# Optimization experiments

Measured on AMD Instinct MI355X. Metric: run time of the kernel, lower is better.

The kernel has to match this reference:

```python
import jax, jax.numpy as jnp
import numpy as np

NUM_GROUPS = 32
EPS = 1e-6


def group_norm(x, gamma, beta):
    # x: [b, c, h, w]
    b, c, h, w = x.shape
    g = NUM_GROUPS
    xg = x.reshape(b, g, c // g, h, w)
    mean = jnp.mean(xg, axis=(2, 3, 4), keepdims=True)
    var = jnp.var(xg, axis=(2, 3, 4), keepdims=True)
    xg = (xg - mean) * jax.lax.rsqrt(var + EPS)
    x = xg.reshape(b, c, h, w)
    return x * gamma[None, :, None, None] + beta[None, :, None, None]


def conv1x1(x, w, bias):
    # x: [b, c_in, h, w], w: [c_out, c_in], bias: [c_out]
    return jnp.einsum('bihw,oi->bohw', x, w) + bias[None, :, None, None]


def setup_inputs() -> dict:
    key = jax.random.key(0)
    ks = jax.random.split(key, 10)
    c = 512
    b, h, w = 4, 64, 64
    scale = 1.0 / np.sqrt(c)
    inp = {
        'x': jax.random.normal(ks[0], (b, c, h, w), dtype=jnp.float32),
        'gn_gamma': jnp.ones((c,), dtype=jnp.float32),
        'gn_beta': jnp.zeros((c,), dtype=jnp.float32),
        'wq': jax.random.normal(ks[1], (c, c), dtype=jnp.float32) * scale,
        'bq': jnp.zeros((c,), dtype=jnp.float32),
        'wk': jax.random.normal(ks[2], (c, c), dtype=jnp.float32) * scale,
        'bk': jnp.zeros((c,), dtype=jnp.float32),
        'wv': jax.random.normal(ks[3], (c, c), dtype=jnp.float32) * scale,
        'bv': jnp.zeros((c,), dtype=jnp.float32),
        'wo': jax.random.normal(ks[4], (c, c), dtype=jnp.float32) * scale,
        'bo': jnp.zeros((c,), dtype=jnp.float32),
    }
    return inp


def reference(x, gn_gamma, gn_beta, wq, bq, wk, bk, wv, bv, wo, bo):
    b, c, h, w = x.shape
    h_ = group_norm(x, gn_gamma, gn_beta)
    q = conv1x1(h_, wq, bq)
    k = conv1x1(h_, wk, bk)
    v = conv1x1(h_, wv, bv)
    n = h * w
    q = q.reshape(b, c, n).transpose(0, 2, 1)  # [b, n, c]
    k = k.reshape(b, c, n)                      # [b, c, n]
    v = v.reshape(b, c, n).transpose(0, 2, 1)  # [b, n, c]
    sim = jnp.einsum('bqc,bck->bqk', q, k) * (c ** -0.5)  # [b, n, n]
    attn = jax.nn.softmax(sim, axis=-1)
    out = jnp.einsum('bqk,bkc->bqc', attn, v)  # [b, n, c]
    out = out.transpose(0, 2, 1).reshape(b, c, h, w)
    out = conv1x1(out, wo, bo)
    return x + out
```

## Files before the change

### kernel.cpp

```cpp
#include <hip/hip_runtime.h>


typedef __attribute__((ext_vector_type(8))) short bf16x8;
typedef __attribute__((ext_vector_type(4))) float f32x4;

#define MFMA16(a, b, c) __builtin_amdgcn_mfma_f32_16x16x32_bf16((a), (b), (c), 0, 0, 0)

#define B_   4
#define C_   512
#define N_   4096
#define SCALE 0.044194173824159216f
#define ESHIFT 12.0f
#define SC2   0.06376297465050853f
#define ES2   17.312340490667562f

__device__ __forceinline__ unsigned short f2bf(float f) {
    union { float f; unsigned int u; } v; v.f = f;
    unsigned int r = (v.u + 0x7fffu + ((v.u >> 16) & 1u)) >> 16;
    return (unsigned short)r;
}
__device__ __forceinline__ float bf2f(unsigned short s) {
    union { unsigned int u; float f; } v; v.u = ((unsigned int)s) << 16;
    return v.f;
}

__device__ __forceinline__ void async16(const unsigned short* g, unsigned short* l) {
    __builtin_amdgcn_global_load_lds((const __attribute__((address_space(1))) unsigned int*)g,
                                     (__attribute__((address_space(3))) unsigned int*)l,
                                     16, 0, 0);
}

__global__ __launch_bounds__(256) void gn_partial(const float* __restrict__ x,
                                                  float* __restrict__ part) {
    int blk = blockIdx.x;
    int gid = blk >> 2, qtr = blk & 3;
    const float4* base = (const float4*)(x + (size_t)gid * 65536) + qtr * 4096;
    float s = 0.f, ss = 0.f;
    for (int i = threadIdx.x; i < 4096; i += 256) {
        float4 v = base[i];
        s  += v.x + v.y + v.z + v.w;
        ss += v.x * v.x + v.y * v.y + v.z * v.z + v.w * v.w;
    }
    __shared__ float red[512];
    int t = threadIdx.x;
    red[t] = s; red[256 + t] = ss;
    __syncthreads();
    for (int st = 128; st > 0; st >>= 1) {
        if (t < st) { red[t] += red[t + st]; red[256 + t] += red[256 + t + st]; }
        __syncthreads();
    }
    if (t == 0) { part[blk] = red[0]; part[512 + blk] = red[256]; }
}

__global__ __launch_bounds__(256) void gn_apply(const float* __restrict__ x,
                                                const float* __restrict__ gamma,
                                                const float* __restrict__ beta,
                                                const float* __restrict__ part,
                                                unsigned short* __restrict__ ht) {
    __shared__ float tile[64][65];
    __shared__ float mrs[4][2];
    int j0 = blockIdx.x * 64, c0 = blockIdx.y * 64, b = blockIdx.z;
    int t = threadIdx.x;
    if (t < 4) {
        int gid = b * 32 + (c0 >> 4) + t;
        float s = 0.f, ss = 0.f;
#pragma unroll
        for (int q = 0; q < 4; ++q) { s += part[gid * 4 + q]; ss += part[512 + gid * 4 + q]; }
        float mean = s * (1.f / 65536.f);
        float var  = ss * (1.f / 65536.f) - mean * mean;
        mrs[t][0] = mean;
        mrs[t][1] = rsqrtf(var + 1e-6f);
    }
    __syncthreads();
#pragma unroll
    for (int i = 0; i < 16; ++i) {
        int lid = i * 256 + t;
        int cl = lid >> 6, jl = lid & 63;
        int c = c0 + cl;
        float v = x[((size_t)b * C_ + c) * N_ + j0 + jl];
        tile[cl][jl] = (v - mrs[cl >> 4][0]) * mrs[cl >> 4][1] * gamma[c] + beta[c];
    }
    __syncthreads();
#pragma unroll
    for (int i = 0; i < 16; ++i) {
        int lid = i * 256 + t;
        int jl = lid >> 6, cl = lid & 63;
        ht[((size_t)b * N_ + j0 + jl) * C_ + c0 + cl] = f2bf(tile[cl][jl]);
    }
}

__global__ __launch_bounds__(256) void wconv(const float* __restrict__ wq,
                                             const float* __restrict__ wk,
                                             const float* __restrict__ wv,
                                             const float* __restrict__ wo,
                                             unsigned short* __restrict__ dst) {
    size_t i = (size_t)blockIdx.x * 256 + threadIdx.x;
    int m = (int)(i >> 18);
    size_t off = i & 262143;
    const float* src = (m == 0) ? wq : (m == 1) ? wk : (m == 2) ? wv : wo;
    dst[i] = f2bf(src[off]);
}

template <typename EPI>
__device__ __forceinline__ void gemm_core(const unsigned short* __restrict__ Abase,
                                          const unsigned short* __restrict__ Bbase,
                                          size_t lda, size_t ldb, int K, EPI epi) {
    __shared__ unsigned short hl[2][128 * 64];
    __shared__ unsigned short wl[2][128 * 64];
    int t = threadIdx.x;
    int wv = t >> 6, lane = t & 63, l15 = lane & 15, quad = lane >> 4;
    int wm = wv & 1, wn = wv >> 1;
    int srow = lane >> 3;
    int sch  = ((lane & 7) ^ srow) * 8;
    int xr = l15 & 7;
    f32x4 acc[4][4] = {};
#pragma unroll
    for (int i = 0; i < 4; ++i) {
        int seg = wv * 4 + i;
        size_t row = seg * 8 + srow;
        async16(&Abase[row * lda + sch], &hl[0][seg * 512]);
        async16(&Bbase[row * ldb + sch], &wl[0][seg * 512]);
    }
    int nk = K >> 6;
    for (int k = 0; k < nk; ++k) {
        int cur = k & 1;
        __builtin_amdgcn_s_waitcnt(0x3F70);
        __syncthreads();
        if (k + 1 < nk) {
            int k0 = (k + 1) << 6;
#pragma unroll
            for (int i = 0; i < 4; ++i) {
                int seg = wv * 4 + i;
                size_t row = seg * 8 + srow;
                async16(&Abase[row * lda + k0 + sch], &hl[cur ^ 1][seg * 512]);
                async16(&Bbase[row * ldb + k0 + sch], &wl[cur ^ 1][seg * 512]);
            }
        }
#pragma unroll
        for (int kk = 0; kk < 2; ++kk) {
            int sl = (((kk << 2) + quad) ^ xr) * 8;
            bf16x8 af[4], bfr[4];
#pragma unroll
            for (int mi = 0; mi < 4; ++mi)
                af[mi] = *(const bf16x8*)&hl[cur][(wm * 64 + mi * 16 + l15) * 64 + sl];
#pragma unroll
            for (int ni = 0; ni < 4; ++ni)
                bfr[ni] = *(const bf16x8*)&wl[cur][(wn * 64 + ni * 16 + l15) * 64 + sl];
#pragma unroll
            for (int mi = 0; mi < 4; ++mi)
#pragma unroll
                for (int ni = 0; ni < 4; ++ni)
                    acc[mi][ni] = MFMA16(af[mi], bfr[ni], acc[mi][ni]);
        }
    }
    epi(acc, wm, wn, l15, quad);
}

__global__ __launch_bounds__(256) void gemm_qkv(const unsigned short* __restrict__ Ht,
                                                const unsigned short* __restrict__ Wb,
                                                const float* __restrict__ bq,
                                                const float* __restrict__ bk,
                                                const float* __restrict__ bv,
                                                unsigned short* __restrict__ Qt,
                                                unsigned short* __restrict__ Kt,
                                                unsigned short* __restrict__ Vg) {
    int b = blockIdx.z, j0 = blockIdx.x * 128;
    int ct = blockIdx.y;
    int slab = ct >> 2, co0 = (ct & 3) * 128;
    const unsigned short* A = Ht + ((size_t)b * N_ + j0) * C_;
    const unsigned short* B = Wb + (size_t)slab * C_ * C_ + (size_t)co0 * C_;
    const float* bias = (slab == 0) ? bq : (slab == 1) ? bk : bv;
    unsigned short* outqk = (slab == 0) ? Qt : Kt;
    gemm_core(A, B, C_, C_, C_,
        [&](f32x4 (&acc)[4][4], int wm, int wn, int l15, int quad) {
        if (slab < 2) {
#pragma unroll
            for (int mi = 0; mi < 4; ++mi)
#pragma unroll
                for (int ni = 0; ni < 4; ++ni)
#pragma unroll
                    for (int r = 0; r < 4; ++r) {
                        int mrow = wm * 64 + mi * 16 + quad * 4 + r;
                        int ncol = wn * 64 + ni * 16 + l15;
                        outqk[((size_t)b * N_ + j0 + mrow) * C_ + co0 + ncol] =
                            f2bf(acc[mi][ni][r] + bias[co0 + ncol]);
                    }
        } else {
#pragma unroll
            for (int mi = 0; mi < 4; ++mi)
#pragma unroll
                for (int ni = 0; ni < 4; ++ni) {
                    int ncol = wn * 64 + ni * 16 + l15;
                    float bb = bias[co0 + ncol];
                    ushort4 pk;
                    pk.x = f2bf(acc[mi][ni][0] + bb);
                    pk.y = f2bf(acc[mi][ni][1] + bb);
                    pk.z = f2bf(acc[mi][ni][2] + bb);
                    pk.w = f2bf(acc[mi][ni][3] + bb);
                    int jb = j0 + wm * 64 + mi * 16 + quad * 4;
                    *(ushort4*)&Vg[((size_t)b * C_ + co0 + ncol) * N_ + jb] = pk;
                }
        }
    });
}

__global__ __launch_bounds__(512, 2) void gemm_qk_exp(const unsigned short* __restrict__ Qt,
                                                      const unsigned short* __restrict__ Kt,
                                                      unsigned short* __restrict__ P,
                                                      float* __restrict__ psum) {
    extern __shared__ unsigned short sm[];
    int lin = blockIdx.x + 16 * blockIdx.y + 256 * blockIdx.z;
    int xcd = lin & 7;
    int i4  = lin >> 3;
    int idx = i4 & 31;
    int b   = i4 >> 5;
    int rq  = xcd & 3, rk = xcd >> 2;
    int j0  = (rq * 4 + (idx & 3)) * 256;
    int ky  = rk * 8 + (idx >> 2);
    int kc0 = ky * 256;
    const unsigned short* A  = Qt + ((size_t)b * N_ + j0) * C_;
    const unsigned short* Bm = Kt + ((size_t)b * N_ + kc0) * C_;

    int t = threadIdx.x;
    int w = t >> 6, lane = t & 63, l15 = lane & 15, quad = lane >> 4;
    int wm = w >> 2, wn = w & 3;
    int srow = lane >> 2;
    int sch  = (((lane & 3) ^ ((lane >> 3) & 3))) * 8;
    int slotq = (quad ^ ((l15 >> 1) & 3)) * 8;

    f32x4 acc[8][4] = {};

    const int NT = 16;
#pragma unroll
    for (int tt = 0; tt < 3; ++tt) {
        unsigned short* dst = sm + (tt << 14);
        size_t k0 = (size_t)tt << 5;
#pragma unroll
        for (int i = 0; i < 2; ++i) {
            int seg = w * 2 + i;
            size_t row = (size_t)seg * 16 + srow;
            async16(&A [row * C_ + k0 + sch], dst + seg * 512);
            async16(&Bm[row * C_ + k0 + sch], dst + 8192 + seg * 512);
        }
    }
    __builtin_amdgcn_s_waitcnt(0x3F78);
    __builtin_amdgcn_s_barrier();

    for (int tt = 0; tt < NT; ++tt) {
        const unsigned short* bp = sm + ((tt & 3) << 14);
        unsigned short* stg = sm + (((tt + 3) & 3) << 14);
        const bool dostage = (tt + 3 < NT);
        size_t k0n = (size_t)(tt + 3) << 5;
        bf16x8 bfr[4], af[4], af2[4];
#pragma unroll
        for (int ni = 0; ni < 4; ++ni)
            bfr[ni] = *(const bf16x8*)&bp[8192 + (wn * 64 + ni * 16 + l15) * 32 + slotq];
#pragma unroll
        for (int mi = 0; mi < 4; ++mi)
            af[mi] = *(const bf16x8*)&bp[(wm * 128 + mi * 16 + l15) * 32 + slotq];
        if (dostage) {
#pragma unroll
            for (int i = 0; i < 2; ++i) {
                int seg = w * 2 + i;
                size_t row = (size_t)seg * 16 + srow;
                async16(&A[row * C_ + k0n + sch], stg + seg * 512);
            }
        }
        __builtin_amdgcn_s_setprio(1);
#pragma unroll
        for (int mi = 0; mi < 4; ++mi)
#pragma unroll
            for (int ni = 0; ni < 4; ++ni)
                acc[mi][ni] = MFMA16(af[mi], bfr[ni], acc[mi][ni]);
        __builtin_amdgcn_s_setprio(0);
#pragma unroll
        for (int mi = 0; mi < 4; ++mi)
            af2[mi] = *(const bf16x8*)&bp[(wm * 128 + (mi + 4) * 16 + l15) * 32 + slotq];
        if (dostage) {
#pragma unroll
            for (int i = 0; i < 2; ++i) {
                int seg = w * 2 + i;
                size_t row = (size_t)seg * 16 + srow;
                async16(&Bm[row * C_ + k0n + sch], stg + 8192 + seg * 512);
            }
        }
        __builtin_amdgcn_s_setprio(1);
#pragma unroll
        for (int mi = 0; mi < 4; ++mi)
#pragma unroll
            for (int ni = 0; ni < 4; ++ni)
                acc[4 + mi][ni] = MFMA16(af2[mi], bfr[ni], acc[4 + mi][ni]);
        __builtin_amdgcn_s_setprio(0);
        if (tt + 1 < NT) {
            if (tt < NT - 3)       __builtin_amdgcn_s_waitcnt(0x3F78);
            else if (tt == NT - 3) __builtin_amdgcn_s_waitcnt(0x3F74);
            else                   __builtin_amdgcn_s_waitcnt(0x3F70);
            __builtin_amdgcn_s_barrier();
        }
    }

#pragma unroll
    for (int mi = 0; mi < 8; ++mi) {
        float rs[4] = {0.f, 0.f, 0.f, 0.f};
#pragma unroll
        for (int ni = 0; ni < 4; ++ni) {
            int ncol = kc0 + wn * 64 + ni * 16 + l15;
#pragma unroll
            for (int r = 0; r < 4; ++r) {
                int mrow = j0 + wm * 128 + mi * 16 + quad * 4 + r;
                float p = exp2f(__builtin_fmaf(acc[mi][ni][r], SC2, -ES2));
                rs[r] += p;
                P[((size_t)b * N_ + mrow) * N_ + ncol] = f2bf(p);
            }
        }
#pragma unroll
        for (int r = 0; r < 4; ++r) {
            float v = rs[r];
            v += __shfl_xor(v, 1);
            v += __shfl_xor(v, 2);
            v += __shfl_xor(v, 4);
            v += __shfl_xor(v, 8);
            if (l15 == 0)
                psum[(size_t)(wn * 16 + ky) * 16384 +
                     (size_t)b * N_ + j0 + wm * 128 + mi * 16 + quad * 4 + r] = v;
        }
    }
}

__global__ __launch_bounds__(512, 2) void gemm_pv(const unsigned short* __restrict__ P,
                                                  const unsigned short* __restrict__ Vg,
                                                  const float* __restrict__ psum,
                                                  unsigned short* __restrict__ ao) {
    extern __shared__ unsigned short sm[];
    __shared__ float linv[256];
    int lin = blockIdx.x;
    int xcd = lin & 7;
    int i4  = lin >> 3;
    int ct  = i4 & 3;
    int grp = xcd + 8 * (i4 >> 2);
    int b = grp & 3, qtile = grp >> 2;
    int j0 = qtile * 256, co0 = ct * 128;
    int t = threadIdx.x;
    int w = t >> 6, lane = t & 63, l15 = lane & 15, quad = lane >> 4;
    int wm = w >> 1, wn = w & 1;
    int srow = lane >> 2;
    int sch  = ((lane & 3) ^ ((lane >> 3) & 3)) * 8;
    int slotq = (quad ^ ((l15 >> 1) & 3)) * 8;
    const unsigned short* A  = P  + ((size_t)b * N_ + j0) * N_;
    const unsigned short* Bm = Vg + ((size_t)b * C_ + co0) * N_;
    f32x4 acc[4][4] = {};
    const int NT = 128;
#pragma unroll
    for (int tt = 0; tt < 3; ++tt) {
        unsigned short* dst = sm + tt * 12288;
        size_t k0 = (size_t)tt << 5;
#pragma unroll
        for (int i = 0; i < 2; ++i) {
            int seg = w * 2 + i;
            size_t row = (size_t)seg * 16 + srow;
            async16(&A[row * N_ + k0 + sch], dst + seg * 512);
        }
        {
            size_t row = (size_t)w * 16 + srow;
            async16(&Bm[row * N_ + k0 + sch], dst + 8192 + w * 512);
        }
    }
    if (t < 256) {
        size_t q = (size_t)b * N_ + j0 + t;
        float s = 0.f;
#pragma unroll
        for (int i = 0; i < 64; ++i) s += psum[(size_t)i * 16384 + q];
        linv[t] = 1.f / s;
    }
    __builtin_amdgcn_s_waitcnt(0x3F76);
    __builtin_amdgcn_s_barrier();
    for (int tt = 0; tt < NT; ++tt) {
        const unsigned short* bp = sm + (tt & 3) * 12288;
        bf16x8 af[4], bfr[4];
#pragma unroll
        for (int mi = 0; mi < 4; ++mi)
            af[mi] = *(const bf16x8*)&bp[(wm * 64 + mi * 16 + l15) * 32 + slotq];
#pragma unroll
        for (int ni = 0; ni < 4; ++ni)
            bfr[ni] = *(const bf16x8*)&bp[8192 + (wn * 64 + ni * 16 + l15) * 32 + slotq];
        if (tt + 3 < NT) {
            unsigned short* stg = sm + ((tt + 3) & 3) * 12288;
            size_t k0n = (size_t)(tt + 3) << 5;
#pragma unroll
            for (int i = 0; i < 2; ++i) {
                int seg = w * 2 + i;
                size_t row = (size_t)seg * 16 + srow;
                async16(&A[row * N_ + k0n + sch], stg + seg * 512);
            }
            {
                size_t row = (size_t)w * 16 + srow;
                async16(&Bm[row * N_ + k0n + sch], stg + 8192 + w * 512);
            }
        }
        __builtin_amdgcn_s_setprio(1);
#pragma unroll
        for (int mi = 0; mi < 4; ++mi)
#pragma unroll
            for (int ni = 0; ni < 4; ++ni)
                acc[mi][ni] = MFMA16(af[mi], bfr[ni], acc[mi][ni]);
        __builtin_amdgcn_s_setprio(0);
        if (tt + 1 < NT) {
            if (tt + 3 < NT)      __builtin_amdgcn_s_waitcnt(0x3F76);
            else if (tt + 2 < NT) __builtin_amdgcn_s_waitcnt(0x3F73);
            else                  __builtin_amdgcn_s_waitcnt(0x3F70);
            __builtin_amdgcn_s_barrier();
        }
    }
#pragma unroll
    for (int mi = 0; mi < 4; ++mi)
#pragma unroll
        for (int ni = 0; ni < 4; ++ni)
#pragma unroll
            for (int r = 0; r < 4; ++r) {
                int mrow = wm * 64 + mi * 16 + quad * 4 + r;
                int ncol = wn * 64 + ni * 16 + l15;
                ao[((size_t)b * N_ + j0 + mrow) * C_ + co0 + ncol] =
                    f2bf(acc[mi][ni][r] * linv[mrow]);
            }
}

__global__ __launch_bounds__(256) void gemm_resid(const unsigned short* __restrict__ AObf,
                                                  const unsigned short* __restrict__ Wo,
                                                  const float* __restrict__ bo,
                                                  const float* __restrict__ xres,
                                                  float* __restrict__ out) {
    int b = blockIdx.z, j0 = blockIdx.x * 128, co0 = blockIdx.y * 128;
    const unsigned short* A = AObf + ((size_t)b * N_ + j0) * C_;
    const unsigned short* B = Wo + (size_t)co0 * C_;
    gemm_core(A, B, C_, C_, C_,
        [&](f32x4 (&acc)[4][4], int wm, int wn, int l15, int quad) {
#pragma unroll
        for (int mi = 0; mi < 4; ++mi)
#pragma unroll
            for (int ni = 0; ni < 4; ++ni) {
                int ncol = wn * 64 + ni * 16 + l15;
                int jb = j0 + wm * 64 + mi * 16 + quad * 4;
                size_t o = ((size_t)b * C_ + co0 + ncol) * N_ + jb;
                float bb = bo[co0 + ncol];
                float4 xr = *(const float4*)&xres[o];
                float4 ov;
                ov.x = acc[mi][ni][0] + bb + xr.x;
                ov.y = acc[mi][ni][1] + bb + xr.y;
                ov.z = acc[mi][ni][2] + bb + xr.z;
                ov.w = acc[mi][ni][3] + bb + xr.w;
                *(float4*)&out[o] = ov;
            }
    });
}

__global__ __launch_bounds__(256, 1) void flash_attn(const unsigned short* __restrict__ Qt,
                                                     const unsigned short* __restrict__ Kt,
                                                     const unsigned short* __restrict__ Vg,
                                                     unsigned short* __restrict__ part,
                                                     float* __restrict__ lbuf,
                                                     int nsplit) {
    extern __shared__ unsigned short smem[];
    unsigned short* Kl = smem;
    unsigned short* Vl = smem + 32768;
    unsigned short* Pl = smem + 65536;

    int flat = blockIdx.x;
    int qblk, b, s;
    if (nsplit == 2) { s = flat & 1; b = (flat >> 1) & 3; qblk = flat >> 3; }
    else             { s = 0;        b = flat & 3;        qblk = flat >> 2; }
    int q0 = qblk * 128;
    int t = threadIdx.x, w = t >> 6, lane = t & 63, l15 = lane & 15, quad = lane >> 4;
    int klen = N_ / nsplit, kbeg = s * klen, nkt = klen / 32;
    int xr = l15 & 7;

    const unsigned short* Kbase = Kt + (size_t)b * N_ * C_;
    const unsigned short* Vbase = Vg + (size_t)b * C_ * N_;

    bf16x8 qa[2][16];
#pragma unroll
    for (int u = 0; u < 2; ++u) {
        const unsigned short* qb =
            Qt + ((size_t)b * N_ + q0 + w * 32 + u * 16 + l15) * C_ + quad * 8;
#pragma unroll
        for (int ck = 0; ck < 16; ++ck) qa[u][ck] = *(const bf16x8*)(qb + ck * 32);
    }

    f32x4 o[2][32] = {};
    float lrow[2][4] = {};

    {
        int k0 = kbeg;
#pragma unroll
        for (int i = 0; i < 8; ++i) {
            int r = w * 8 + i;
            async16(Kbase + (size_t)(k0 + r) * C_ + ((lane ^ (r & 7)) * 8), Kl + r * 512);
        }
#pragma unroll
        for (int i = 0; i < 8; ++i) {
            int idx = w * 8 + i, kc = idx >> 3, cb = idx & 7;
            async16(Vbase + (size_t)(cb * 64 + lane) * N_ + k0 + kc * 8,
                    Vl + (kc * 512 + cb * 64) * 8);
        }
    }

    for (int kt = 0; kt < nkt; ++kt) {
        int cur = kt & 1, nxt = cur ^ 1;
        __builtin_amdgcn_s_waitcnt(0x3F70);
        __syncthreads();
        if (kt + 1 < nkt) {
            int k0 = kbeg + (kt + 1) * 32;
#pragma unroll
            for (int i = 0; i < 8; ++i) {
                int r = w * 8 + i;
                async16(Kbase + (size_t)(k0 + r) * C_ + ((lane ^ (r & 7)) * 8),
                        Kl + nxt * 16384 + r * 512);
            }
#pragma unroll
            for (int i = 0; i < 8; ++i) {
                int idx = w * 8 + i, kc = idx >> 3, cb = idx & 7;
                async16(Vbase + (size_t)(cb * 64 + lane) * N_ + k0 + kc * 8,
                        Vl + nxt * 16384 + (kc * 512 + cb * 64) * 8);
            }
        }
        const unsigned short* Kc = Kl + cur * 16384;
        f32x4 s00 = {}, s01 = {}, s10 = {}, s11 = {};
#pragma unroll
        for (int ck = 0; ck < 16; ++ck) {
            int slot = (ck * 4 + quad) ^ xr;
            bf16x8 b0 = *(const bf16x8*)&Kc[l15 * 512 + slot * 8];
            bf16x8 b1 = *(const bf16x8*)&Kc[(16 + l15) * 512 + slot * 8];
            s00 = MFMA16(qa[0][ck], b0, s00);
            s10 = MFMA16(qa[1][ck], b0, s10);
            s01 = MFMA16(qa[0][ck], b1, s01);
            s11 = MFMA16(qa[1][ck], b1, s11);
        }
        unsigned short* pb = &Pl[w * 1152];
#pragma unroll
        for (int r = 0; r < 4; ++r) {
            float p00 = __expf(s00[r] * SCALE - ESHIFT);
            float p01 = __expf(s01[r] * SCALE - ESHIFT);
            float p10 = __expf(s10[r] * SCALE - ESHIFT);
            float p11 = __expf(s11[r] * SCALE - ESHIFT);
            lrow[0][r] += p00 + p01;
            lrow[1][r] += p10 + p11;
            int row0 = (quad * 4 + r) * 36;
            int row1 = (16 + quad * 4 + r) * 36;
            pb[row0 + l15]      = f2bf(p00);
            pb[row0 + 16 + l15] = f2bf(p01);
            pb[row1 + l15]      = f2bf(p10);
            pb[row1 + 16 + l15] = f2bf(p11);
        }
        __builtin_amdgcn_s_waitcnt(0xC07F);
        bf16x8 pa0 = *(const bf16x8*)&Pl[w * 1152 + l15 * 36 + quad * 8];
        bf16x8 pa1 = *(const bf16x8*)&Pl[w * 1152 + (16 + l15) * 36 + quad * 8];
        const unsigned short* Vc = Vl + cur * 16384;
#pragma unroll
        for (int cf = 0; cf < 32; ++cf) {
            bf16x8 vb = *(const bf16x8*)&Vc[(quad * 512 + cf * 16 + l15) * 8];
            o[0][cf] = MFMA16(pa0, vb, o[0][cf]);
            o[1][cf] = MFMA16(pa1, vb, o[1][cf]);
        }
    }
#pragma unroll
    for (int u = 0; u < 2; ++u)
#pragma unroll
        for (int r = 0; r < 4; ++r) {
            float l = lrow[u][r];
            l += __shfl_xor(l, 1);
            l += __shfl_xor(l, 2);
            l += __shfl_xor(l, 4);
            l += __shfl_xor(l, 8);
            lrow[u][r] = l;
        }
    size_t pbase = (size_t)(s * B_ + b) * N_;
#pragma unroll
    for (int u = 0; u < 2; ++u)
#pragma unroll
        for (int cf = 0; cf < 32; ++cf)
#pragma unroll
            for (int r = 0; r < 4; ++r) {
                int q = q0 + w * 32 + u * 16 + quad * 4 + r;
                part[(pbase + q) * C_ + cf * 16 + l15] = f2bf(o[u][cf][r]);
            }
    if (l15 == 0) {
#pragma unroll
        for (int u = 0; u < 2; ++u)
#pragma unroll
            for (int r = 0; r < 4; ++r) {
                int q = q0 + w * 32 + u * 16 + quad * 4 + r;
                lbuf[pbase + q] = lrow[u][r];
            }
    }
}

__global__ __launch_bounds__(256) void attn_combine(const unsigned short* __restrict__ part,
                                                    const float* __restrict__ lbuf,
                                                    unsigned short* __restrict__ ao,
                                                    int nsplit) {
    size_t idx = (size_t)blockIdx.x * 256 + threadIdx.x;
    int cu = (int)(idx & 63);
    size_t row = idx >> 6;
    float l = lbuf[row];
    union { uint4 v; unsigned short u[8]; } p1, p2, outv;
    p1.v = *(const uint4*)&part[row * C_ + cu * 8];
    if (nsplit == 2) {
        l += lbuf[(size_t)B_ * N_ + row];
        p2.v = *(const uint4*)&part[((size_t)B_ * N_ + row) * C_ + cu * 8];
    } else {
        p2.v = make_uint4(0, 0, 0, 0);
    }
    float inv = 1.f / l;
#pragma unroll
    for (int j = 0; j < 8; ++j)
        outv.u[j] = f2bf((bf2f(p1.u[j]) + bf2f(p2.u[j])) * inv);
    *(uint4*)&ao[row * C_ + cu * 8] = outv.v;
}

extern "C" void kernel_launch(void* const* d_in, const int* in_sizes, int n_in,
                              void* d_out, int out_size, void* d_ws, size_t ws_size,
                              hipStream_t stream) {
    const float* x   = (const float*)d_in[0];
    const float* gam = (const float*)d_in[1];
    const float* bet = (const float*)d_in[2];
    const float* wq  = (const float*)d_in[3];
    const float* bq  = (const float*)d_in[4];
    const float* wk  = (const float*)d_in[5];
    const float* bk  = (const float*)d_in[6];
    const float* wv  = (const float*)d_in[7];
    const float* bv  = (const float*)d_in[8];
    const float* wo  = (const float*)d_in[9];
    const float* bo  = (const float*)d_in[10];
    float* out = (float*)d_out;

    char* ws = (char*)d_ws;
    const size_t SZH = (size_t)B_ * N_ * C_ * 2;
    const size_t OFF_HT = 4096;
    const size_t OFF_QT = OFF_HT + SZH;
    const size_t OFF_KT = OFF_QT + SZH;
    const size_t OFF_VG = OFF_KT + SZH;
    const size_t OFF_WB = OFF_VG + SZH;
    const size_t OFF_X  = OFF_WB + 2097152;
    float*          part0 = (float*)ws;
    unsigned short* Ht    = (unsigned short*)(ws + OFF_HT);
    unsigned short* Qt    = (unsigned short*)(ws + OFF_QT);
    unsigned short* Kt    = (unsigned short*)(ws + OFF_KT);
    unsigned short* Vg    = (unsigned short*)(ws + OFF_VG);
    unsigned short* Wb    = (unsigned short*)(ws + OFF_WB);
    unsigned short* AObf  = Ht;

    const size_t SZPSUM = 64ull * 16384 * 4;
    const size_t SZP    = (size_t)B_ * N_ * N_ * 2;
    float*          psum = (float*)(ws + OFF_X);
    unsigned short* P    = (unsigned short*)(ws + OFF_X + SZPSUM);
    size_t needA = OFF_X + SZPSUM + SZP;

    float*          lbuf = (float*)(ws + OFF_X);
    unsigned short* partb = (unsigned short*)(ws + OFF_X + 262144);
    size_t needB2 = OFF_X + 262144 + 2 * SZH;

    gn_partial<<<512, 256, 0, stream>>>(x, part0);
    gn_apply<<<dim3(64, 8, B_), 256, 0, stream>>>(x, gam, bet, part0, Ht);
    wconv<<<4096, 256, 0, stream>>>(wq, wk, wv, wo, Wb);
    gemm_qkv<<<dim3(32, 12, B_), 256, 0, stream>>>(Ht, Wb, bq, bk, bv, Qt, Kt, Vg);

    if (ws_size >= needA) {
        const int QK_LDS = 131072;
        (void)hipFuncSetAttribute((const void*)gemm_qk_exp,
                                  hipFuncAttributeMaxDynamicSharedMemorySize, QK_LDS);
        gemm_qk_exp<<<dim3(16, 16, B_), 512, QK_LDS, stream>>>(Qt, Kt, P, psum);
        const int PV_LDS = 98304;
        (void)hipFuncSetAttribute((const void*)gemm_pv,
                                  hipFuncAttributeMaxDynamicSharedMemorySize, PV_LDS);
        gemm_pv<<<256, 512, PV_LDS, stream>>>(P, Vg, psum, AObf);
    } else {
        int nsplit = (ws_size >= needB2) ? 2 : 1;
        const int FLASH_LDS = 140288;
        (void)hipFuncSetAttribute((const void*)flash_attn,
                                  hipFuncAttributeMaxDynamicSharedMemorySize, FLASH_LDS);
        flash_attn<<<dim3(32 * B_ * nsplit), 256, FLASH_LDS, stream>>>(Qt, Kt, Vg, partb, lbuf, nsplit);
        attn_combine<<<4096, 256, 0, stream>>>(partb, lbuf, AObf, nsplit);
    }
    gemm_resid<<<dim3(32, 4, B_), 256, 0, stream>>>(AObf, Wb + 786432, bo, x, out);
}
```

Baseline: 325.4 us.

## Halve barriers in QK and PV GEMM loops via two-stage-per-barrier pipelining

Restructures the main K-loops of the QK^T/exp kernel and the P·V kernel so each iteration processes two k-tiles between block barriers. Prefetch depth drops from 3 tiles ahead to 2, so the 4-slot LDS ring can be reused without a barrier after every tile. The first sub-step only waits on the wave's own async loads, with a sched_barrier in place of the block barrier. This cuts workgroup barrier count in half, at the cost of less prefetch lookahead to hide global load latency.

```diff
diff --git a/kernel.cpp b/kernel.cpp
--- a/kernel.cpp
+++ b/kernel.cpp
@@ -232,7 +232,7 @@
 
     const int NT = 16;
 #pragma unroll
-    for (int tt = 0; tt < 3; ++tt) {
+    for (int tt = 0; tt < 2; ++tt) {
         unsigned short* dst = sm + (tt << 14);
         size_t k0 = (size_t)tt << 5;
 #pragma unroll
@@ -243,58 +243,67 @@
             async16(&Bm[row * C_ + k0 + sch], dst + 8192 + seg * 512);
         }
     }
-    __builtin_amdgcn_s_waitcnt(0x3F78);
+    __builtin_amdgcn_s_waitcnt(0x3F74);
     __builtin_amdgcn_s_barrier();
 
-    for (int tt = 0; tt < NT; ++tt) {
-        const unsigned short* bp = sm + ((tt & 3) << 14);
-        unsigned short* stg = sm + (((tt + 3) & 3) << 14);
-        const bool dostage = (tt + 3 < NT);
-        size_t k0n = (size_t)(tt + 3) << 5;
-        bf16x8 bfr[4], af[4], af2[4];
-#pragma unroll
-        for (int ni = 0; ni < 4; ++ni)
-            bfr[ni] = *(const bf16x8*)&bp[8192 + (wn * 64 + ni * 16 + l15) * 32 + slotq];
-#pragma unroll
-        for (int mi = 0; mi < 4; ++mi)
-            af[mi] = *(const bf16x8*)&bp[(wm * 128 + mi * 16 + l15) * 32 + slotq];
-        if (dostage) {
-#pragma unroll
-            for (int i = 0; i < 2; ++i) {
-                int seg = w * 2 + i;
-                size_t row = (size_t)seg * 16 + srow;
-                async16(&A[row * C_ + k0n + sch], stg + seg * 512);
-            }
-        }
-        __builtin_amdgcn_s_setprio(1);
-#pragma unroll
-        for (int mi = 0; mi < 4; ++mi)
+    for (int tt = 0; tt < NT; tt += 2) {
+#pragma unroll
+        for (int s = 0; s < 2; ++s) {
+            int tc = tt + s;
+            const unsigned short* bp = sm + ((tc & 3) << 14);
+            int ts = tc + 2;
+            unsigned short* stg = sm + ((ts & 3) << 14);
+            const bool dostage = (ts < NT);
+            size_t k0n = (size_t)ts << 5;
+            bf16x8 bfr[4], af[4], af2[4];
 #pragma unroll
             for (int ni = 0; ni < 4; ++ni)
-                acc[mi][ni] = MFMA16(af[mi], bfr[ni], acc[mi][ni]);
-        __builtin_amdgcn_s_setprio(0);
-#pragma unroll
-        for (int mi = 0; mi < 4; ++mi)
-            af2[mi] = *(const bf16x8*)&bp[(wm * 128 + (mi + 4) * 16 + l15) * 32 + slotq];
-        if (dostage) {
-#pragma unroll
-            for (int i = 0; i < 2; ++i) {
-                int seg = w * 2 + i;
-                size_t row = (size_t)seg * 16 + srow;
-                async16(&Bm[row * C_ + k0n + sch], stg + 8192 + seg * 512);
-            }
-        }
-        __builtin_amdgcn_s_setprio(1);
-#pragma unroll
-        for (int mi = 0; mi < 4; ++mi)
-#pragma unroll
-            for (int ni = 0; ni < 4; ++ni)
-                acc[4 + mi][ni] = MFMA16(af2[mi], bfr[ni], acc[4 + mi][ni]);
-        __builtin_amdgcn_s_setprio(0);
-        if (tt + 1 < NT) {
-            if (tt < NT - 3)       __builtin_amdgcn_s_waitcnt(0x3F78);
-            else if (tt == NT - 3) __builtin_amdgcn_s_waitcnt(0x3F74);
-            else                   __builtin_amdgcn_s_waitcnt(0x3F70);
+                bfr[ni] = *(const bf16x8*)&bp[8192 + (wn * 64 + ni * 16 + l15) * 32 + slotq];
+#pragma unroll
+            for (int mi = 0; mi < 4; ++mi)
+                af[mi] = *(const bf16x8*)&bp[(wm * 128 + mi * 16 + l15) * 32 + slotq];
+            if (dostage) {
+#pragma unroll
+                for (int i = 0; i < 2; ++i) {
+                    int seg = w * 2 + i;
+                    size_t row = (size_t)seg * 16 + srow;
+                    async16(&A[row * C_ + k0n + sch], stg + seg * 512);
+                }
+            }
+            __builtin_amdgcn_s_setprio(1);
+#pragma unroll
+            for (int mi = 0; mi < 4; ++mi)
+#pragma unroll
+                for (int ni = 0; ni < 4; ++ni)
+                    acc[mi][ni] = MFMA16(af[mi], bfr[ni], acc[mi][ni]);
+            __builtin_amdgcn_s_setprio(0);
+#pragma unroll
+            for (int mi = 0; mi < 4; ++mi)
+                af2[mi] = *(const bf16x8*)&bp[(wm * 128 + (mi + 4) * 16 + l15) * 32 + slotq];
+            if (dostage) {
+#pragma unroll
+                for (int i = 0; i < 2; ++i) {
+                    int seg = w * 2 + i;
+                    size_t row = (size_t)seg * 16 + srow;
+                    async16(&Bm[row * C_ + k0n + sch], stg + 8192 + seg * 512);
+                }
+            }
+            __builtin_amdgcn_s_setprio(1);
+#pragma unroll
+            for (int mi = 0; mi < 4; ++mi)
+#pragma unroll
+                for (int ni = 0; ni < 4; ++ni)
+                    acc[4 + mi][ni] = MFMA16(af2[mi], bfr[ni], acc[4 + mi][ni]);
+            __builtin_amdgcn_s_setprio(0);
+            if (s == 0) {
+                if (tt + 2 < NT) __builtin_amdgcn_s_waitcnt(0x3F74);
+                else             __builtin_amdgcn_s_waitcnt(0x3F70);
+                __builtin_amdgcn_sched_barrier(0);
+            }
+        }
+        if (tt + 2 < NT) {
+            if (tt + 3 < NT) __builtin_amdgcn_s_waitcnt(0x3F74);
+            else             __builtin_amdgcn_s_waitcnt(0x3F70);
             __builtin_amdgcn_s_barrier();
         }
     }
@@ -351,7 +360,7 @@
     f32x4 acc[4][4] = {};
     const int NT = 128;
 #pragma unroll
-    for (int tt = 0; tt < 3; ++tt) {
+    for (int tt = 0; tt < 2; ++tt) {
         unsigned short* dst = sm + tt * 12288;
         size_t k0 = (size_t)tt << 5;
 #pragma unroll
@@ -372,42 +381,51 @@
         for (int i = 0; i < 64; ++i) s += psum[(size_t)i * 16384 + q];
         linv[t] = 1.f / s;
     }
-    __builtin_amdgcn_s_waitcnt(0x3F76);
+    __builtin_amdgcn_s_waitcnt(0x3F73);
     __builtin_amdgcn_s_barrier();
-    for (int tt = 0; tt < NT; ++tt) {
-        const unsigned short* bp = sm + (tt & 3) * 12288;
-        bf16x8 af[4], bfr[4];
-#pragma unroll
-        for (int mi = 0; mi < 4; ++mi)
-            af[mi] = *(const bf16x8*)&bp[(wm * 64 + mi * 16 + l15) * 32 + slotq];
-#pragma unroll
-        for (int ni = 0; ni < 4; ++ni)
-            bfr[ni] = *(const bf16x8*)&bp[8192 + (wn * 64 + ni * 16 + l15) * 32 + slotq];
-        if (tt + 3 < NT) {
-            unsigned short* stg = sm + ((tt + 3) & 3) * 12288;
-            size_t k0n = (size_t)(tt + 3) << 5;
-#pragma unroll
-            for (int i = 0; i < 2; ++i) {
-                int seg = w * 2 + i;
-                size_t row = (size_t)seg * 16 + srow;
-                async16(&A[row * N_ + k0n + sch], stg + seg * 512);
-            }
-            {
-                size_t row = (size_t)w * 16 + srow;
-                async16(&Bm[row * N_ + k0n + sch], stg + 8192 + w * 512);
-            }
-        }
-        __builtin_amdgcn_s_setprio(1);
-#pragma unroll
-        for (int mi = 0; mi < 4; ++mi)
+    for (int tt = 0; tt < NT; tt += 2) {
+#pragma unroll
+        for (int s = 0; s < 2; ++s) {
+            int tc = tt + s;
+            const unsigned short* bp = sm + (tc & 3) * 12288;
+            int ts = tc + 2;
+            bf16x8 af[4], bfr[4];
+#pragma unroll
+            for (int mi = 0; mi < 4; ++mi)
+                af[mi] = *(const bf16x8*)&bp[(wm * 64 + mi * 16 + l15) * 32 + slotq];
 #pragma unroll
             for (int ni = 0; ni < 4; ++ni)
-                acc[mi][ni] = MFMA16(af[mi], bfr[ni], acc[mi][ni]);
-        __builtin_amdgcn_s_setprio(0);
-        if (tt + 1 < NT) {
-            if (tt + 3 < NT)      __builtin_amdgcn_s_waitcnt(0x3F76);
-            else if (tt + 2 < NT) __builtin_amdgcn_s_waitcnt(0x3F73);
-            else                  __builtin_amdgcn_s_waitcnt(0x3F70);
+                bfr[ni] = *(const bf16x8*)&bp[8192 + (wn * 64 + ni * 16 + l15) * 32 + slotq];
+            if (ts < NT) {
+                unsigned short* stg = sm + (ts & 3) * 12288;
+                size_t k0n = (size_t)ts << 5;
+#pragma unroll
+                for (int i = 0; i < 2; ++i) {
+                    int seg = w * 2 + i;
+                    size_t row = (size_t)seg * 16 + srow;
+                    async16(&A[row * N_ + k0n + sch], stg + seg * 512);
+                }
+                {
+                    size_t row = (size_t)w * 16 + srow;
+                    async16(&Bm[row * N_ + k0n + sch], stg + 8192 + w * 512);
+                }
+            }
+            __builtin_amdgcn_s_setprio(1);
+#pragma unroll
+            for (int mi = 0; mi < 4; ++mi)
+#pragma unroll
+                for (int ni = 0; ni < 4; ++ni)
+                    acc[mi][ni] = MFMA16(af[mi], bfr[ni], acc[mi][ni]);
+            __builtin_amdgcn_s_setprio(0);
+            if (s == 0) {
+                if (tt + 2 < NT) __builtin_amdgcn_s_waitcnt(0x3F73);
+                else             __builtin_amdgcn_s_waitcnt(0x3F70);
+                __builtin_amdgcn_sched_barrier(0);
+            }
+        }
+        if (tt + 2 < NT) {
+            if (tt + 3 < NT) __builtin_amdgcn_s_waitcnt(0x3F73);
+            else             __builtin_amdgcn_s_waitcnt(0x3F70);
             __builtin_amdgcn_s_barrier();
         }
     }
```

Measured after the change: 320.7 us. About the same (-1.4%).
